# Optimization experiments

Hardware: AMD Instinct MI355X
Metric: run time of the kernel (lower is better)

## Reference

```python
import jax, jax.numpy as jnp
import numpy as np

B, N, D, H = 256, 64, 128, 64

def _w(key, shape, fan_in):
    return jax.random.normal(key, shape, jnp.float32) * (1.0 / np.sqrt(fan_in))

def setup_inputs() -> dict:
    key = jax.random.key(0)
    ks = jax.random.split(key, 6)
    return {
        "observations": jax.random.normal(ks[0], (B, N, D), jnp.float32),
        "enc_w": _w(ks[1], (D, H), D), "enc_b": jnp.zeros((H,), jnp.float32),
        "gate_w1": _w(ks[2], (2 * H, H), 2 * H), "gate_b1": jnp.zeros((H,), jnp.float32),
        "gate_w2": _w(ks[3], (H, 1), H), "gate_b2": jnp.zeros((1,), jnp.float32),
        "msg_w1": _w(ks[4], (H, H), H), "msg_b1": jnp.zeros((H,), jnp.float32),
        "msg_w2": _w(ks[5], (H, H), H), "msg_b2": jnp.zeros((H,), jnp.float32),
    }

def reference(observations, enc_w, enc_b, gate_w1, gate_b1, gate_w2, gate_b2,
              msg_w1, msg_b1, msg_w2, msg_b2):
    # encoder: (B, N, H)
    enc = jax.nn.relu(observations @ enc_w + enc_b)
    h = enc.shape[-1]
    # gate layer 1 on concat([e_i, e_j]) == e_i @ W_top + e_j @ W_bot; avoids
    # materializing the (B, N, N, 2H) concat tensor.
    w_i, w_j = gate_w1[:h], gate_w1[h:]
    gi = enc @ w_i                       # (B, N, H) contribution of receiver i
    gj = enc @ w_j + gate_b1             # (B, N, H) contribution of sender j
    hid = jax.nn.relu(gi[:, :, None, :] + gj[:, None, :, :])   # (B, N, N, H)
    gates = jax.nn.sigmoid(jnp.squeeze(hid @ gate_w2, -1) + gate_b2[0])  # (B, N, N)
    # message_gen(encoded): identical for every i in the original loop
    msg = jax.nn.relu(enc @ msg_w1 + msg_b1) @ msg_w2 + msg_b2  # (B, N, H)
    # enhanced[b, i] = sum_j gates[b, i, j] * msg[b, j]
    enhanced = jnp.einsum('bij,bjh->bih', gates, msg)           # (B, N, H)
    return enhanced
```

## Files before the change

kernel.cpp:

```cpp
#include <hip/hip_runtime.h>

typedef float  f32x4  __attribute__((ext_vector_type(4)));
typedef short  bf16x8 __attribute__((ext_vector_type(8)));

#define Bb 256

__device__ __forceinline__ uint cvtpk(float lo, float hi) {
    uint r;
    asm("v_cvt_pk_bf16_f32 %0, %1, %2" : "=v"(r) : "v"(lo), "v"(hi));
    return r;
}
__device__ __forceinline__ ushort f2b1(float v) { return (ushort)cvtpk(v, v); }
__device__ __forceinline__ float bflo(uint u) { return __uint_as_float(u << 16); }
__device__ __forceinline__ float bfhi(uint u) { return __uint_as_float(u & 0xffff0000u); }

__device__ __forceinline__ void gl_lds16(const void* g, void* l) {
    __builtin_amdgcn_global_load_lds(
        (const __attribute__((address_space(1))) unsigned int*)g,
        (__attribute__((address_space(3))) unsigned int*)l, 16, 0, 0);
}

union U8 { uint u[4]; bf16x8 v; };

__global__ __launch_bounds__(256) void gcm_prep(
    const float* __restrict__ obs, const float* __restrict__ enc_w,
    const float* __restrict__ gate_w1, const float* __restrict__ msg_w1,
    const float* __restrict__ msg_w2,
    ushort* __restrict__ obs_bf, ushort* __restrict__ wimg)
{
    const int bid = blockIdx.x, t = threadIdx.x;
    if (bid < 1024) {
        const int G  = bid * 256 + t;
        const int e0 = G * 8;
        const int b  = e0 >> 13;
        const int r  = (e0 >> 7) & 63;
        const int d0 = e0 & 127;
        const int ds = d0 ^ ((r & 7) << 3);
        const float* src = obs + (((size_t)b * 64 + r) * 128 + ds);
        float4 f0 = *(const float4*)src;
        float4 f1 = *(const float4*)(src + 4);
        uint4 o;
        o.x = cvtpk(f0.x, f0.y); o.y = cvtpk(f0.z, f0.w);
        o.z = cvtpk(f1.x, f1.y); o.w = cvtpk(f1.z, f1.w);
        *(uint4*)(obs_bf + e0) = o;
    } else {
        const int G  = (bid - 1024) * 256 + t;
        const int e0 = G * 8;
        float v[8];
        if (e0 < 8192) {
            const int n  = e0 >> 7;
            const int k0 = (e0 & 127) ^ ((n & 7) << 3);
            #pragma unroll
            for (int j = 0; j < 8; ++j) v[j] = enc_w[(k0 + j) * 64 + n];
        } else {
            const int e  = e0 - 8192;
            const int n  = e >> 6;
            const int k0 = (e & 63) ^ ((n & 7) << 3);
            const float* base; int col;
            if (n < 64)       { base = gate_w1;           col = n;       }
            else if (n < 128) { base = gate_w1 + 64 * 64; col = n - 64;  }
            else if (n < 192) { base = msg_w1;            col = n - 128; }
            else              { base = msg_w2;            col = n - 192; }
            #pragma unroll
            for (int j = 0; j < 8; ++j) v[j] = base[(k0 + j) * 64 + col];
        }
        uint4 o;
        o.x = cvtpk(v[0], v[1]); o.y = cvtpk(v[2], v[3]);
        o.z = cvtpk(v[4], v[5]); o.w = cvtpk(v[6], v[7]);
        *(uint4*)(wimg + e0) = o;
    }
}

__global__ __launch_bounds__(512, 4) void gcm_main(
    const ushort* __restrict__ obs_bf, const ushort* __restrict__ wimg,
    const float* __restrict__ enc_b, const float* __restrict__ gate_b1,
    const float* __restrict__ gate_w2, const float* __restrict__ gate_b2,
    const float* __restrict__ msg_b1, const float* __restrict__ msg_b2,
    ushort* __restrict__ gi_ws, float* __restrict__ out)
{
    const int bid  = blockIdx.x;
    const int bb   = bid >> 1;
    const int half = bid & 1;
    const int t    = threadIdx.x;
    const int lane = t & 63;
    const int wv   = t >> 6;
    const int lr   = lane & 15;
    const int lg   = lane >> 4;
    const int rt   = wv & 3;
    const int ch   = wv >> 2;

    __shared__ __align__(16) char arena[61440];
    ushort* s_wT     = (ushort*)(arena);
    ushort* s_enc    = (ushort*)(arena + 32768);
    ushort* s_msgT   = (ushort*)(arena + 32768);
    ushort* s_msgh   = (ushort*)(arena + 40960);
    ushort* s_gjb    = (ushort*)(arena + 49152);
    ushort* s_gatesb = (ushort*)(arena + 57344);

    #pragma unroll
    for (int i = 0; i < 4; ++i) {
        const int idx = wv * 4 + i;
        gl_lds16(wimg + 8192 + idx * 512 + lane * 8, arena + idx * 1024);
    }

    {
        const int arow = rt * 16 + lr;
        const ushort* ob = obs_bf + (size_t)bb * 8192 + arow * 128;
        bf16x8 a[4];
        #pragma unroll
        for (int ks = 0; ks < 4; ++ks)
            a[ks] = *(const bf16x8*)(ob + ((ks * 32 + lg * 8) ^ ((arow & 7) << 3)));
        f32x4 acc[2];
        acc[0] = (f32x4){0.f, 0.f, 0.f, 0.f};
        acc[1] = (f32x4){0.f, 0.f, 0.f, 0.f};
        #pragma unroll
        for (int jj = 0; jj < 2; ++jj) {
            const int n = ch * 32 + jj * 16 + lr;
            const ushort* wp = wimg + n * 128;
            #pragma unroll
            for (int ks = 0; ks < 4; ++ks) {
                bf16x8 bw = *(const bf16x8*)(wp + ((ks * 32 + lg * 8) ^ ((n & 7) << 3)));
                acc[jj] = __builtin_amdgcn_mfma_f32_16x16x32_bf16(a[ks], bw, acc[jj], 0, 0, 0);
            }
        }
        const int rb = rt * 16 + lg * 4;
        #pragma unroll
        for (int jj = 0; jj < 2; ++jj) {
            const int n = ch * 32 + jj * 16 + lr;
            const float be = enc_b[n];
            float v0 = fmaxf(acc[jj][0] + be, 0.f), v1 = fmaxf(acc[jj][1] + be, 0.f);
            float v2 = fmaxf(acc[jj][2] + be, 0.f), v3 = fmaxf(acc[jj][3] + be, 0.f);
            uint pA = cvtpk(v0, v1), pB = cvtpk(v2, v3);
            s_enc[((rb + 0) * 64 + n) ^ (((rb + 0) & 7) << 3)] = (ushort)pA;
            s_enc[((rb + 1) * 64 + n) ^ (((rb + 1) & 7) << 3)] = (ushort)(pA >> 16);
            s_enc[((rb + 2) * 64 + n) ^ (((rb + 2) & 7) << 3)] = (ushort)pB;
            s_enc[((rb + 3) * 64 + n) ^ (((rb + 3) & 7) << 3)] = (ushort)(pB >> 16);
        }
    }
    __syncthreads();

    {
        const int arow = rt * 16 + lr;
        bf16x8 a2[2];
        #pragma unroll
        for (int ks = 0; ks < 2; ++ks)
            a2[ks] = *(const bf16x8*)(s_enc + ((arow * 64 + ks * 32 + lg * 8) ^ ((arow & 7) << 3)));
        f32x4 acc[6];
        #pragma unroll
        for (int q = 0; q < 6; ++q) acc[q] = (f32x4){0.f, 0.f, 0.f, 0.f};
        #pragma unroll
        for (int q = 0; q < 6; ++q) {
            const int n = (ch * 6 + q) * 16 + lr;
            #pragma unroll
            for (int ks = 0; ks < 2; ++ks) {
                bf16x8 bw = *(const bf16x8*)(s_wT + ((n * 64 + ks * 32 + lg * 8) ^ ((n & 7) << 3)));
                acc[q] = __builtin_amdgcn_mfma_f32_16x16x32_bf16(a2[ks], bw, acc[q], 0, 0, 0);
            }
        }
        const int rb = rt * 16 + lg * 4;
        #pragma unroll
        for (int q = 0; q < 6; ++q) {
            const int nfull = (ch * 6 + q) * 16;
            const int cc = nfull + lr;
            if (nfull < 64) {
                if ((rt >> 1) == half) {
                    #pragma unroll
                    for (int rr = 0; rr < 4; ++rr)
                        gi_ws[(size_t)bb * 4096 + (rb + rr) * 64 + cc] = f2b1(acc[q][rr]);
                }
            } else if (nfull < 128) {
                const float b1 = gate_b1[cc - 64];
                #pragma unroll
                for (int rr = 0; rr < 4; ++rr) {
                    const int row = rb + rr;
                    s_gjb[(row * 64 + (cc - 64)) ^ ((row & 7) << 3)] = f2b1(acc[q][rr] + b1);
                }
            } else {
                const float bm = msg_b1[cc - 128];
                float v0 = fmaxf(acc[q][0] + bm, 0.f), v1 = fmaxf(acc[q][1] + bm, 0.f);
                float v2 = fmaxf(acc[q][2] + bm, 0.f), v3 = fmaxf(acc[q][3] + bm, 0.f);
                uint pA = cvtpk(v0, v1), pB = cvtpk(v2, v3);
                const int c2 = cc - 128;
                s_msgh[((rb + 0) * 64 + c2) ^ (((rb + 0) & 7) << 3)] = (ushort)pA;
                s_msgh[((rb + 1) * 64 + c2) ^ (((rb + 1) & 7) << 3)] = (ushort)(pA >> 16);
                s_msgh[((rb + 2) * 64 + c2) ^ (((rb + 2) & 7) << 3)] = (ushort)pB;
                s_msgh[((rb + 3) * 64 + c2) ^ (((rb + 3) & 7) << 3)] = (ushort)(pB >> 16);
            }
        }
    }
    __syncthreads();

    {
        const int arow = rt * 16 + lr;
        bf16x8 a3[2];
        #pragma unroll
        for (int ks = 0; ks < 2; ++ks)
            a3[ks] = *(const bf16x8*)(s_msgh + ((arow * 64 + ks * 32 + lg * 8) ^ ((arow & 7) << 3)));
        #pragma unroll
        for (int jj = 0; jj < 2; ++jj) {
            const int n = 192 + ch * 32 + jj * 16 + lr;
            f32x4 acc = (f32x4){0.f, 0.f, 0.f, 0.f};
            #pragma unroll
            for (int ks = 0; ks < 2; ++ks) {
                bf16x8 bw = *(const bf16x8*)(s_wT + ((n * 64 + ks * 32 + lg * 8) ^ ((n & 7) << 3)));
                acc = __builtin_amdgcn_mfma_f32_16x16x32_bf16(a3[ks], bw, acc, 0, 0, 0);
            }
            const int h  = ch * 32 + jj * 16 + lr;
            const int jb = rt * 16 + lg * 4;
            const float bm2 = msg_b2[h];
            uint pA = cvtpk(acc[0] + bm2, acc[1] + bm2);
            uint pB = cvtpk(acc[2] + bm2, acc[3] + bm2);
            const int e = (h * 64 + jb) ^ ((h & 7) << 3);
            *(uint*)(s_msgT + e)     = pA;
            *(uint*)(s_msgT + e + 2) = pB;
        }
    }

    {
        const int lrow0 = wv * 4;
        float gjv[64];
        #pragma unroll
        for (int c8 = 0; c8 < 8; ++c8) {
            uint4 p = *(const uint4*)(s_gjb + ((lane * 64 + c8 * 8) ^ ((lane & 7) << 3)));
            gjv[c8 * 8 + 0] = bflo(p.x); gjv[c8 * 8 + 1] = bfhi(p.x);
            gjv[c8 * 8 + 2] = bflo(p.y); gjv[c8 * 8 + 3] = bfhi(p.y);
            gjv[c8 * 8 + 4] = bflo(p.z); gjv[c8 * 8 + 5] = bfhi(p.z);
            gjv[c8 * 8 + 6] = bflo(p.w); gjv[c8 * 8 + 7] = bfhi(p.w);
        }
        const float b2v = gate_b2[0];
        #pragma unroll
        for (int r = 0; r < 4; ++r) {
            const int lrow = lrow0 + r;
            const int grow = __builtin_amdgcn_readfirstlane(half * 32 + lrow);
            const uint* gip = (const uint*)(gi_ws + (size_t)bb * 4096 + grow * 64);
            float acc = 0.f;
            #pragma unroll
            for (int c = 0; c < 32; ++c) {
                const uint p = gip[c];
                acc = fmaf(fmaxf(bflo(p) + gjv[2 * c],     0.f), gate_w2[2 * c],     acc);
                acc = fmaf(fmaxf(bfhi(p) + gjv[2 * c + 1], 0.f), gate_w2[2 * c + 1], acc);
            }
            const float g = 1.f / (1.f + __expf(-(acc + b2v)));
            s_gatesb[(lrow * 64 + lane) ^ ((lrow & 7) << 3)] = f2b1(g);
        }
    }
    __syncthreads();

    {
        const int rtl = wv >> 2;
        const int ctl = wv & 3;
        f32x4 acc = (f32x4){0.f, 0.f, 0.f, 0.f};
        const int arow = rtl * 16 + lr;
        const int n = ctl * 16 + lr;
        #pragma unroll
        for (int ks = 0; ks < 2; ++ks) {
            const int k0 = ks * 32 + lg * 8;
            bf16x8 a5 = *(const bf16x8*)(s_gatesb + ((arow * 64 + k0) ^ ((arow & 7) << 3)));
            bf16x8 b5 = *(const bf16x8*)(s_msgT   + ((n * 64 + k0) ^ ((n & 7) << 3)));
            acc = __builtin_amdgcn_mfma_f32_16x16x32_bf16(a5, b5, acc, 0, 0, 0);
        }
        const int rb = half * 32 + rtl * 16 + lg * 4;
        #pragma unroll
        for (int rr = 0; rr < 4; ++rr)
            out[((size_t)bb * 64 + rb + rr) * 64 + n] = acc[rr];
    }
}

__global__ __launch_bounds__(1024) void gcm_fb(
    const float* __restrict__ obs, const float* __restrict__ enc_w,
    const float* __restrict__ enc_b, const float* __restrict__ gate_w1,
    const float* __restrict__ gate_b1, const float* __restrict__ gate_w2,
    const float* __restrict__ gate_b2, const float* __restrict__ msg_w1,
    const float* __restrict__ msg_b1, const float* __restrict__ msg_w2,
    const float* __restrict__ msg_b2, float* __restrict__ out)
{
    const int bb   = blockIdx.x;
    const int t    = threadIdx.x;
    const int lane = t & 63;
    const int wv   = t >> 6;
    const int lr   = lane & 15;
    const int lg   = lane >> 4;
    const int rt   = wv & 3;
    const int ct   = wv >> 2;

    __shared__ __align__(16) ushort s_encwT[64 * 128];
    __shared__ __align__(16) ushort s_wT[256 * 64];
    __shared__ __align__(16) ushort s_enc[64 * 64];
    __shared__ __align__(16) ushort s_msgh[64 * 64];
    __shared__ __align__(16) ushort s_gatesb[64 * 64];
    __shared__ __align__(16) ushort s_msgT[64 * 64];
    __shared__ __align__(16) float  s_gi[64 * 64];
    __shared__ __align__(16) float  s_gj[64 * 64];
    __shared__ __align__(16) float  s_w2[64];

    float4 pf[8];
    {
        const float* ob = obs + ((size_t)bb * 64 + rt * 16 + lr) * 128 + lg * 8;
        #pragma unroll
        for (int ks = 0; ks < 4; ++ks) {
            pf[2 * ks]     = *(const float4*)(ob + ks * 32);
            pf[2 * ks + 1] = *(const float4*)(ob + ks * 32 + 4);
        }
    }
    if (t < 64) s_w2[t] = gate_w2[t];
    #pragma unroll
    for (int it = 0; it < 2; ++it) {
        const int g  = t + it * 1024;
        const int k  = g >> 4;
        const int n0 = (g & 15) * 4;
        float4 w4 = *(const float4*)(enc_w + k * 64 + n0);
        uint pA = cvtpk(w4.x, w4.y), pB = cvtpk(w4.z, w4.w);
        s_encwT[((n0 + 0) * 128 + k) ^ (((n0 + 0) & 7) << 3)] = (ushort)pA;
        s_encwT[((n0 + 1) * 128 + k) ^ (((n0 + 1) & 7) << 3)] = (ushort)(pA >> 16);
        s_encwT[((n0 + 2) * 128 + k) ^ (((n0 + 2) & 7) << 3)] = (ushort)pB;
        s_encwT[((n0 + 3) * 128 + k) ^ (((n0 + 3) & 7) << 3)] = (ushort)(pB >> 16);
    }
    bf16x8 afrag[4];
    #pragma unroll
    for (int ks = 0; ks < 4; ++ks) {
        U8 u;
        u.u[0] = cvtpk(pf[2 * ks].x,     pf[2 * ks].y);
        u.u[1] = cvtpk(pf[2 * ks].z,     pf[2 * ks].w);
        u.u[2] = cvtpk(pf[2 * ks + 1].x, pf[2 * ks + 1].y);
        u.u[3] = cvtpk(pf[2 * ks + 1].z, pf[2 * ks + 1].w);
        afrag[ks] = u.v;
    }
    float4 pfw[4];
    {
        const int k  = t >> 4;
        const int n0 = (t & 15) * 4;
        pfw[0] = *(const float4*)(gate_w1 + k * 64 + n0);
        pfw[1] = *(const float4*)(gate_w1 + (64 + k) * 64 + n0);
        pfw[2] = *(const float4*)(msg_w1 + k * 64 + n0);
        pfw[3] = *(const float4*)(msg_w2 + k * 64 + n0);
    }
    __syncthreads();
    {
        f32x4 acc = (f32x4){0.f, 0.f, 0.f, 0.f};
        const int n = ct * 16 + lr;
        #pragma unroll
        for (int ks = 0; ks < 4; ++ks) {
            const int k0 = ks * 32 + lg * 8;
            bf16x8 bf = *(const bf16x8*)(s_encwT + ((n * 128 + k0) ^ ((n & 7) << 3)));
            acc = __builtin_amdgcn_mfma_f32_16x16x32_bf16(afrag[ks], bf, acc, 0, 0, 0);
        }
        #pragma unroll
        for (int it = 0; it < 4; ++it) {
            const int k  = t >> 4;
            const int n0 = it * 64 + (t & 15) * 4;
            uint pA = cvtpk(pfw[it].x, pfw[it].y), pB = cvtpk(pfw[it].z, pfw[it].w);
            s_wT[((n0 + 0) * 64 + k) ^ (((n0 + 0) & 7) << 3)] = (ushort)pA;
            s_wT[((n0 + 1) * 64 + k) ^ (((n0 + 1) & 7) << 3)] = (ushort)(pA >> 16);
            s_wT[((n0 + 2) * 64 + k) ^ (((n0 + 2) & 7) << 3)] = (ushort)pB;
            s_wT[((n0 + 3) * 64 + k) ^ (((n0 + 3) & 7) << 3)] = (ushort)(pB >> 16);
        }
        const float be = enc_b[n];
        float v0 = fmaxf(acc[0] + be, 0.f), v1 = fmaxf(acc[1] + be, 0.f);
        float v2 = fmaxf(acc[2] + be, 0.f), v3 = fmaxf(acc[3] + be, 0.f);
        uint pA = cvtpk(v0, v1), pB = cvtpk(v2, v3);
        const int rb = rt * 16 + lg * 4;
        s_enc[((rb + 0) * 64 + n) ^ (((rb + 0) & 7) << 3)] = (ushort)pA;
        s_enc[((rb + 1) * 64 + n) ^ (((rb + 1) & 7) << 3)] = (ushort)(pA >> 16);
        s_enc[((rb + 2) * 64 + n) ^ (((rb + 2) & 7) << 3)] = (ushort)pB;
        s_enc[((rb + 3) * 64 + n) ^ (((rb + 3) & 7) << 3)] = (ushort)(pB >> 16);
    }
    __syncthreads();
    {
        f32x4 acc[3];
        #pragma unroll
        for (int q = 0; q < 3; ++q) acc[q] = (f32x4){0.f, 0.f, 0.f, 0.f};
        const int arow = rt * 16 + lr;
        #pragma unroll
        for (int ks = 0; ks < 2; ++ks) {
            const int k0 = ks * 32 + lg * 8;
            bf16x8 a = *(const bf16x8*)(s_enc + ((arow * 64 + k0) ^ ((arow & 7) << 3)));
            #pragma unroll
            for (int q = 0; q < 3; ++q) {
                const int n = (ct * 3 + q) * 16 + lr;
                bf16x8 bf = *(const bf16x8*)(s_wT + ((n * 64 + k0) ^ ((n & 7) << 3)));
                acc[q] = __builtin_amdgcn_mfma_f32_16x16x32_bf16(a, bf, acc[q], 0, 0, 0);
            }
        }
        const int rb = rt * 16 + lg * 4;
        #pragma unroll
        for (int q = 0; q < 3; ++q) {
            const int nfull = (ct * 3 + q) * 16;
            const int cc = nfull + lr;
            if (nfull < 64) {
                #pragma unroll
                for (int rr = 0; rr < 4; ++rr) {
                    const int row = rb + rr;
                    s_gi[(row * 64 + cc) ^ ((row & 7) << 2)] = acc[q][rr];
                }
            } else if (nfull < 128) {
                const float b1 = gate_b1[cc - 64];
                #pragma unroll
                for (int rr = 0; rr < 4; ++rr) {
                    const int row = rb + rr;
                    s_gj[(row * 64 + (cc - 64)) ^ ((row & 7) << 2)] = acc[q][rr] + b1;
                }
            } else {
                const float bm = msg_b1[cc - 128];
                float v0 = fmaxf(acc[q][0] + bm, 0.f), v1 = fmaxf(acc[q][1] + bm, 0.f);
                float v2 = fmaxf(acc[q][2] + bm, 0.f), v3 = fmaxf(acc[q][3] + bm, 0.f);
                uint pA = cvtpk(v0, v1), pB = cvtpk(v2, v3);
                const int c2 = cc - 128;
                s_msgh[((rb + 0) * 64 + c2) ^ (((rb + 0) & 7) << 3)] = (ushort)pA;
                s_msgh[((rb + 1) * 64 + c2) ^ (((rb + 1) & 7) << 3)] = (ushort)(pA >> 16);
                s_msgh[((rb + 2) * 64 + c2) ^ (((rb + 2) & 7) << 3)] = (ushort)pB;
                s_msgh[((rb + 3) * 64 + c2) ^ (((rb + 3) & 7) << 3)] = (ushort)(pB >> 16);
            }
        }
    }
    __syncthreads();
    {
        f32x4 acc = (f32x4){0.f, 0.f, 0.f, 0.f};
        const int arow = rt * 16 + lr;
        const int nn3 = 192 + ct * 16 + lr;
        #pragma unroll
        for (int ks = 0; ks < 2; ++ks) {
            const int k0 = ks * 32 + lg * 8;
            bf16x8 a = *(const bf16x8*)(s_msgh + ((arow * 64 + k0) ^ ((arow & 7) << 3)));
            bf16x8 bf = *(const bf16x8*)(s_wT + ((nn3 * 64 + k0) ^ ((nn3 & 7) << 3)));
            acc = __builtin_amdgcn_mfma_f32_16x16x32_bf16(a, bf, acc, 0, 0, 0);
        }
        const int h  = ct * 16 + lr;
        const int jb = rt * 16 + lg * 4;
        const float bm2 = msg_b2[h];
        uint pA = cvtpk(acc[0] + bm2, acc[1] + bm2);
        uint pB = cvtpk(acc[2] + bm2, acc[3] + bm2);
        const int e = (h * 64 + jb) ^ ((h & 7) << 3);
        *(uint*)(s_msgT + e)     = pA;
        *(uint*)(s_msgT + e + 2) = pB;
    }
    {
        const int row0g = wv * 4;
        float ag[4] = {0.f, 0.f, 0.f, 0.f};
        #pragma unroll 4
        for (int h0 = 0; h0 < 64; h0 += 4) {
            float4 gj4 = *(const float4*)&s_gj[(lane * 64 + h0) ^ ((lane & 7) << 2)];
            float4 w24 = *(const float4*)&s_w2[h0];
            #pragma unroll
            for (int r = 0; r < 4; ++r) {
                const int row = row0g + r;
                float4 gi4 = *(const float4*)&s_gi[(row * 64 + h0) ^ ((row & 7) << 2)];
                ag[r] = fmaf(fmaxf(gi4.x + gj4.x, 0.f), w24.x, ag[r]);
                ag[r] = fmaf(fmaxf(gi4.y + gj4.y, 0.f), w24.y, ag[r]);
                ag[r] = fmaf(fmaxf(gi4.z + gj4.z, 0.f), w24.z, ag[r]);
                ag[r] = fmaf(fmaxf(gi4.w + gj4.w, 0.f), w24.w, ag[r]);
            }
        }
        const float b2v = gate_b2[0];
        #pragma unroll
        for (int r = 0; r < 4; ++r) {
            const int row = row0g + r;
            const float g = 1.f / (1.f + __expf(-(ag[r] + b2v)));
            s_gatesb[(row * 64 + lane) ^ ((row & 7) << 3)] = f2b1(g);
        }
    }
    __syncthreads();
    {
        const int rtl = wv >> 2;
        const int ctl = wv & 3;
        f32x4 acc = (f32x4){0.f, 0.f, 0.f, 0.f};
        const int arow = rtl * 16 + lr;
        const int n = ctl * 16 + lr;
        #pragma unroll
        for (int ks = 0; ks < 2; ++ks) {
            const int k0 = ks * 32 + lg * 8;
            bf16x8 a  = *(const bf16x8*)(s_gatesb + ((arow * 64 + k0) ^ ((arow & 7) << 3)));
            bf16x8 bf = *(const bf16x8*)(s_msgT   + ((n * 64 + k0) ^ ((n & 7) << 3)));
            acc = __builtin_amdgcn_mfma_f32_16x16x32_bf16(a, bf, acc, 0, 0, 0);
        }
        const int rb = rtl * 16 + lg * 4;
        #pragma unroll
        for (int rr = 0; rr < 4; ++rr)
            out[((size_t)bb * 64 + rb + rr) * 64 + n] = acc[rr];
    }
}

extern "C" void kernel_launch(void* const* d_in, const int* in_sizes, int n_in,
                              void* d_out, int out_size, void* d_ws, size_t ws_size,
                              hipStream_t stream) {
    const float* obs     = (const float*)d_in[0];
    const float* enc_w   = (const float*)d_in[1];
    const float* enc_b   = (const float*)d_in[2];
    const float* gate_w1 = (const float*)d_in[3];
    const float* gate_b1 = (const float*)d_in[4];
    const float* gate_w2 = (const float*)d_in[5];
    const float* gate_b2 = (const float*)d_in[6];
    const float* msg_w1  = (const float*)d_in[7];
    const float* msg_b1  = (const float*)d_in[8];
    const float* msg_w2  = (const float*)d_in[9];
    const float* msg_b2  = (const float*)d_in[10];
    float* out = (float*)d_out;

    const size_t obs_elems = (size_t)Bb * 64 * 128;
    const size_t w_elems   = 24576;
    const size_t gi_elems  = (size_t)Bb * 64 * 64;
    const size_t need = (obs_elems + w_elems + gi_elems) * sizeof(ushort);
    if (ws_size >= need) {
        ushort* obs_bf = (ushort*)d_ws;
        ushort* wimg   = obs_bf + obs_elems;
        ushort* gi_ws  = wimg + w_elems;
        gcm_prep<<<1036, 256, 0, stream>>>(obs, enc_w, gate_w1, msg_w1, msg_w2,
                                           obs_bf, wimg);
        gcm_main<<<2 * Bb, 512, 0, stream>>>(obs_bf, wimg, enc_b, gate_b1,
                                             gate_w2, gate_b2, msg_b1, msg_b2,
                                             gi_ws, out);
    } else {
        gcm_fb<<<Bb, 1024, 0, stream>>>(obs, enc_w, enc_b, gate_w1, gate_b1,
                                        gate_w2, gate_b2, msg_w1, msg_b1,
                                        msg_w2, msg_b2, out);
    }
}
```

Measured before the change: 22.43 us.

## Restructure main kernel to one block per batch with wave-private row tiles

The main kernel now launches one 256-thread block per batch instead of two 512-thread half-blocks. Each wave owns 16 rows end to end, keeping intermediates in wave-private LDS. This removes the redundant per-half recompute, the global gi workspace round trip, the LDS weight staging, and all but one block barrier. Weights are now read straight from global memory/cache, each wave issues more MFMAs serially, and there are half as many blocks, which may reduce parallelism and latency hiding.

```diff
diff --git a/kernel.cpp b/kernel.cpp
--- a/kernel.cpp
+++ b/kernel.cpp
@@ -13,12 +13,6 @@
 __device__ __forceinline__ ushort f2b1(float v) { return (ushort)cvtpk(v, v); }
 __device__ __forceinline__ float bflo(uint u) { return __uint_as_float(u << 16); }
 __device__ __forceinline__ float bfhi(uint u) { return __uint_as_float(u & 0xffff0000u); }
-
-__device__ __forceinline__ void gl_lds16(const void* g, void* l) {
-    __builtin_amdgcn_global_load_lds(
-        (const __attribute__((address_space(1))) unsigned int*)g,
-        (__attribute__((address_space(3))) unsigned int*)l, 16, 0, 0);
-}
 
 union U8 { uint u[4]; bf16x8 v; };
 
@@ -71,142 +65,125 @@
     }
 }
 
-__global__ __launch_bounds__(512, 4) void gcm_main(
+__global__ __launch_bounds__(256) void gcm_main(
     const ushort* __restrict__ obs_bf, const ushort* __restrict__ wimg,
     const float* __restrict__ enc_b, const float* __restrict__ gate_b1,
     const float* __restrict__ gate_w2, const float* __restrict__ gate_b2,
     const float* __restrict__ msg_b1, const float* __restrict__ msg_b2,
-    ushort* __restrict__ gi_ws, float* __restrict__ out)
+    float* __restrict__ out)
 {
-    const int bid  = blockIdx.x;
-    const int bb   = bid >> 1;
-    const int half = bid & 1;
+    const int bb   = blockIdx.x;
     const int t    = threadIdx.x;
     const int lane = t & 63;
     const int wv   = t >> 6;
     const int lr   = lane & 15;
     const int lg   = lane >> 4;
-    const int rt   = wv & 3;
-    const int ch   = wv >> 2;
-
-    __shared__ __align__(16) char arena[61440];
-    ushort* s_wT     = (ushort*)(arena);
-    ushort* s_enc    = (ushort*)(arena + 32768);
-    ushort* s_msgT   = (ushort*)(arena + 32768);
-    ushort* s_msgh   = (ushort*)(arena + 40960);
-    ushort* s_gjb    = (ushort*)(arena + 49152);
-    ushort* s_gatesb = (ushort*)(arena + 57344);
-
-    #pragma unroll
-    for (int i = 0; i < 4; ++i) {
-        const int idx = wv * 4 + i;
-        gl_lds16(wimg + 8192 + idx * 512 + lane * 8, arena + idx * 1024);
-    }
-
-    {
-        const int arow = rt * 16 + lr;
+    const int R0   = wv * 16;
+
+    __shared__ __align__(16) char arena[41984];
+    ushort* s_pr1 = (ushort*)(arena)         + wv * 1024;
+    ushort* s_gi  = (ushort*)(arena + 8192)  + wv * 1024;
+    ushort* s_gat = (ushort*)(arena + 16384) + wv * 1024;
+    ushort* s_gjb  = (ushort*)(arena + 24576);
+    ushort* s_msgT = (ushort*)(arena + 33792);
+
+    {
+        const int arow = R0 + lr;
         const ushort* ob = obs_bf + (size_t)bb * 8192 + arow * 128;
         bf16x8 a[4];
         #pragma unroll
         for (int ks = 0; ks < 4; ++ks)
             a[ks] = *(const bf16x8*)(ob + ((ks * 32 + lg * 8) ^ ((arow & 7) << 3)));
-        f32x4 acc[2];
-        acc[0] = (f32x4){0.f, 0.f, 0.f, 0.f};
-        acc[1] = (f32x4){0.f, 0.f, 0.f, 0.f};
-        #pragma unroll
-        for (int jj = 0; jj < 2; ++jj) {
-            const int n = ch * 32 + jj * 16 + lr;
+        f32x4 acc[4];
+        #pragma unroll
+        for (int ct = 0; ct < 4; ++ct) acc[ct] = (f32x4){0.f, 0.f, 0.f, 0.f};
+        #pragma unroll
+        for (int ct = 0; ct < 4; ++ct) {
+            const int n = ct * 16 + lr;
             const ushort* wp = wimg + n * 128;
             #pragma unroll
             for (int ks = 0; ks < 4; ++ks) {
                 bf16x8 bw = *(const bf16x8*)(wp + ((ks * 32 + lg * 8) ^ ((n & 7) << 3)));
-                acc[jj] = __builtin_amdgcn_mfma_f32_16x16x32_bf16(a[ks], bw, acc[jj], 0, 0, 0);
-            }
-        }
-        const int rb = rt * 16 + lg * 4;
-        #pragma unroll
-        for (int jj = 0; jj < 2; ++jj) {
-            const int n = ch * 32 + jj * 16 + lr;
+                acc[ct] = __builtin_amdgcn_mfma_f32_16x16x32_bf16(a[ks], bw, acc[ct], 0, 0, 0);
+            }
+        }
+        #pragma unroll
+        for (int ct = 0; ct < 4; ++ct) {
+            const int n = ct * 16 + lr;
             const float be = enc_b[n];
-            float v0 = fmaxf(acc[jj][0] + be, 0.f), v1 = fmaxf(acc[jj][1] + be, 0.f);
-            float v2 = fmaxf(acc[jj][2] + be, 0.f), v3 = fmaxf(acc[jj][3] + be, 0.f);
-            uint pA = cvtpk(v0, v1), pB = cvtpk(v2, v3);
-            s_enc[((rb + 0) * 64 + n) ^ (((rb + 0) & 7) << 3)] = (ushort)pA;
-            s_enc[((rb + 1) * 64 + n) ^ (((rb + 1) & 7) << 3)] = (ushort)(pA >> 16);
-            s_enc[((rb + 2) * 64 + n) ^ (((rb + 2) & 7) << 3)] = (ushort)pB;
-            s_enc[((rb + 3) * 64 + n) ^ (((rb + 3) & 7) << 3)] = (ushort)(pB >> 16);
-        }
-    }
-    __syncthreads();
-
-    {
-        const int arow = rt * 16 + lr;
+            #pragma unroll
+            for (int rr = 0; rr < 4; ++rr) {
+                const int row = lg * 4 + rr;
+                float v = fmaxf(acc[ct][rr] + be, 0.f);
+                s_pr1[(row * 64 + n) ^ ((row & 7) << 3)] = f2b1(v);
+            }
+        }
+    }
+
+    {
         bf16x8 a2[2];
         #pragma unroll
         for (int ks = 0; ks < 2; ++ks)
-            a2[ks] = *(const bf16x8*)(s_enc + ((arow * 64 + ks * 32 + lg * 8) ^ ((arow & 7) << 3)));
-        f32x4 acc[6];
-        #pragma unroll
-        for (int q = 0; q < 6; ++q) acc[q] = (f32x4){0.f, 0.f, 0.f, 0.f};
-        #pragma unroll
-        for (int q = 0; q < 6; ++q) {
-            const int n = (ch * 6 + q) * 16 + lr;
+            a2[ks] = *(const bf16x8*)(s_pr1 + ((lr * 64 + ks * 32 + lg * 8) ^ ((lr & 7) << 3)));
+        f32x4 acc[12];
+        #pragma unroll
+        for (int q = 0; q < 12; ++q) acc[q] = (f32x4){0.f, 0.f, 0.f, 0.f};
+        #pragma unroll
+        for (int q = 0; q < 12; ++q) {
+            const int n = q * 16 + lr;
+            const ushort* wp = wimg + 8192 + n * 64;
             #pragma unroll
             for (int ks = 0; ks < 2; ++ks) {
-                bf16x8 bw = *(const bf16x8*)(s_wT + ((n * 64 + ks * 32 + lg * 8) ^ ((n & 7) << 3)));
+                bf16x8 bw = *(const bf16x8*)(wp + ((ks * 32 + lg * 8) ^ ((n & 7) << 3)));
                 acc[q] = __builtin_amdgcn_mfma_f32_16x16x32_bf16(a2[ks], bw, acc[q], 0, 0, 0);
             }
         }
-        const int rb = rt * 16 + lg * 4;
-        #pragma unroll
-        for (int q = 0; q < 6; ++q) {
-            const int nfull = (ch * 6 + q) * 16;
+        #pragma unroll
+        for (int q = 0; q < 12; ++q) {
+            const int nfull = q * 16;
             const int cc = nfull + lr;
             if (nfull < 64) {
-                if ((rt >> 1) == half) {
-                    #pragma unroll
-                    for (int rr = 0; rr < 4; ++rr)
-                        gi_ws[(size_t)bb * 4096 + (rb + rr) * 64 + cc] = f2b1(acc[q][rr]);
+                #pragma unroll
+                for (int rr = 0; rr < 4; ++rr) {
+                    const int row = lg * 4 + rr;
+                    s_gi[(row * 64 + cc) ^ ((row & 7) << 3)] = f2b1(acc[q][rr]);
                 }
             } else if (nfull < 128) {
                 const float b1 = gate_b1[cc - 64];
                 #pragma unroll
                 for (int rr = 0; rr < 4; ++rr) {
-                    const int row = rb + rr;
-                    s_gjb[(row * 64 + (cc - 64)) ^ ((row & 7) << 3)] = f2b1(acc[q][rr] + b1);
+                    const int grow = R0 + lg * 4 + rr;
+                    s_gjb[grow * 72 + (cc - 64)] = f2b1(acc[q][rr] + b1);
                 }
             } else {
                 const float bm = msg_b1[cc - 128];
-                float v0 = fmaxf(acc[q][0] + bm, 0.f), v1 = fmaxf(acc[q][1] + bm, 0.f);
-                float v2 = fmaxf(acc[q][2] + bm, 0.f), v3 = fmaxf(acc[q][3] + bm, 0.f);
-                uint pA = cvtpk(v0, v1), pB = cvtpk(v2, v3);
-                const int c2 = cc - 128;
-                s_msgh[((rb + 0) * 64 + c2) ^ (((rb + 0) & 7) << 3)] = (ushort)pA;
-                s_msgh[((rb + 1) * 64 + c2) ^ (((rb + 1) & 7) << 3)] = (ushort)(pA >> 16);
-                s_msgh[((rb + 2) * 64 + c2) ^ (((rb + 2) & 7) << 3)] = (ushort)pB;
-                s_msgh[((rb + 3) * 64 + c2) ^ (((rb + 3) & 7) << 3)] = (ushort)(pB >> 16);
-            }
-        }
-    }
-    __syncthreads();
-
-    {
-        const int arow = rt * 16 + lr;
+                #pragma unroll
+                for (int rr = 0; rr < 4; ++rr) {
+                    const int row = lg * 4 + rr;
+                    float v = fmaxf(acc[q][rr] + bm, 0.f);
+                    s_pr1[(row * 64 + (cc - 128)) ^ ((row & 7) << 3)] = f2b1(v);
+                }
+            }
+        }
+    }
+
+    {
         bf16x8 a3[2];
         #pragma unroll
         for (int ks = 0; ks < 2; ++ks)
-            a3[ks] = *(const bf16x8*)(s_msgh + ((arow * 64 + ks * 32 + lg * 8) ^ ((arow & 7) << 3)));
-        #pragma unroll
-        for (int jj = 0; jj < 2; ++jj) {
-            const int n = 192 + ch * 32 + jj * 16 + lr;
+            a3[ks] = *(const bf16x8*)(s_pr1 + ((lr * 64 + ks * 32 + lg * 8) ^ ((lr & 7) << 3)));
+        #pragma unroll
+        for (int jj = 0; jj < 4; ++jj) {
+            const int n = 192 + jj * 16 + lr;
+            const ushort* wp = wimg + 8192 + n * 64;
             f32x4 acc = (f32x4){0.f, 0.f, 0.f, 0.f};
             #pragma unroll
             for (int ks = 0; ks < 2; ++ks) {
-                bf16x8 bw = *(const bf16x8*)(s_wT + ((n * 64 + ks * 32 + lg * 8) ^ ((n & 7) << 3)));
+                bf16x8 bw = *(const bf16x8*)(wp + ((ks * 32 + lg * 8) ^ ((n & 7) << 3)));
                 acc = __builtin_amdgcn_mfma_f32_16x16x32_bf16(a3[ks], bw, acc, 0, 0, 0);
             }
-            const int h  = ch * 32 + jj * 16 + lr;
-            const int jb = rt * 16 + lg * 4;
+            const int h  = jj * 16 + lr;
+            const int jb = R0 + lg * 4;
             const float bm2 = msg_b2[h];
             uint pA = cvtpk(acc[0] + bm2, acc[1] + bm2);
             uint pB = cvtpk(acc[2] + bm2, acc[3] + bm2);
@@ -216,12 +193,13 @@
         }
     }
 
-    {
-        const int lrow0 = wv * 4;
+    __syncthreads();
+
+    {
         float gjv[64];
         #pragma unroll
         for (int c8 = 0; c8 < 8; ++c8) {
-            uint4 p = *(const uint4*)(s_gjb + ((lane * 64 + c8 * 8) ^ ((lane & 7) << 3)));
+            uint4 p = *(const uint4*)(s_gjb + lane * 72 + c8 * 8);
             gjv[c8 * 8 + 0] = bflo(p.x); gjv[c8 * 8 + 1] = bfhi(p.x);
             gjv[c8 * 8 + 2] = bflo(p.y); gjv[c8 * 8 + 3] = bfhi(p.y);
             gjv[c8 * 8 + 4] = bflo(p.z); gjv[c8 * 8 + 5] = bfhi(p.z);
@@ -229,40 +207,46 @@
         }
         const float b2v = gate_b2[0];
         #pragma unroll
-        for (int r = 0; r < 4; ++r) {
-            const int lrow = lrow0 + r;
-            const int grow = __builtin_amdgcn_readfirstlane(half * 32 + lrow);
-            const uint* gip = (const uint*)(gi_ws + (size_t)bb * 4096 + grow * 64);
+        for (int i = 0; i < 16; ++i) {
             float acc = 0.f;
             #pragma unroll
-            for (int c = 0; c < 32; ++c) {
-                const uint p = gip[c];
-                acc = fmaf(fmaxf(bflo(p) + gjv[2 * c],     0.f), gate_w2[2 * c],     acc);
-                acc = fmaf(fmaxf(bfhi(p) + gjv[2 * c + 1], 0.f), gate_w2[2 * c + 1], acc);
+            for (int c8 = 0; c8 < 8; ++c8) {
+                uint4 p = *(const uint4*)(s_gi + ((i * 64 + c8 * 8) ^ ((i & 7) << 3)));
+                const float* w2p = gate_w2 + c8 * 8;
+                acc = fmaf(fmaxf(bflo(p.x) + gjv[c8 * 8 + 0], 0.f), w2p[0], acc);
+                acc = fmaf(fmaxf(bfhi(p.x) + gjv[c8 * 8 + 1], 0.f), w2p[1], acc);
+                acc = fmaf(fmaxf(bflo(p.y) + gjv[c8 * 8 + 2], 0.f), w2p[2], acc);
+                acc = fmaf(fmaxf(bfhi(p.y) + gjv[c8 * 8 + 3], 0.f), w2p[3], acc);
+                acc = fmaf(fmaxf(bflo(p.z) + gjv[c8 * 8 + 4], 0.f), w2p[4], acc);
+                acc = fmaf(fmaxf(bfhi(p.z) + gjv[c8 * 8 + 5], 0.f), w2p[5], acc);
+                acc = fmaf(fmaxf(bflo(p.w) + gjv[c8 * 8 + 6], 0.f), w2p[6], acc);
+                acc = fmaf(fmaxf(bfhi(p.w) + gjv[c8 * 8 + 7], 0.f), w2p[7], acc);
             }
             const float g = 1.f / (1.f + __expf(-(acc + b2v)));
-            s_gatesb[(lrow * 64 + lane) ^ ((lrow & 7) << 3)] = f2b1(g);
-        }
-    }
-    __syncthreads();
-
-    {
-        const int rtl = wv >> 2;
-        const int ctl = wv & 3;
-        f32x4 acc = (f32x4){0.f, 0.f, 0.f, 0.f};
-        const int arow = rtl * 16 + lr;
-        const int n = ctl * 16 + lr;
-        #pragma unroll
-        for (int ks = 0; ks < 2; ++ks) {
-            const int k0 = ks * 32 + lg * 8;
-            bf16x8 a5 = *(const bf16x8*)(s_gatesb + ((arow * 64 + k0) ^ ((arow & 7) << 3)));
-            bf16x8 b5 = *(const bf16x8*)(s_msgT   + ((n * 64 + k0) ^ ((n & 7) << 3)));
-            acc = __builtin_amdgcn_mfma_f32_16x16x32_bf16(a5, b5, acc, 0, 0, 0);
-        }
-        const int rb = half * 32 + rtl * 16 + lg * 4;
-        #pragma unroll
-        for (int rr = 0; rr < 4; ++rr)
-            out[((size_t)bb * 64 + rb + rr) * 64 + n] = acc[rr];
+            s_gat[(i * 64 + lane) ^ ((i & 7) << 3)] = f2b1(g);
+        }
+    }
+
+    {
+        bf16x8 a5[2];
+        #pragma unroll
+        for (int ks = 0; ks < 2; ++ks)
+            a5[ks] = *(const bf16x8*)(s_gat + ((lr * 64 + ks * 32 + lg * 8) ^ ((lr & 7) << 3)));
+        #pragma unroll
+        for (int ctl = 0; ctl < 4; ++ctl) {
+            const int n = ctl * 16 + lr;
+            f32x4 acc = (f32x4){0.f, 0.f, 0.f, 0.f};
+            #pragma unroll
+            for (int ks = 0; ks < 2; ++ks) {
+                bf16x8 b5 = *(const bf16x8*)(s_msgT + ((n * 64 + ks * 32 + lg * 8) ^ ((n & 7) << 3)));
+                acc = __builtin_amdgcn_mfma_f32_16x16x32_bf16(a5[ks], b5, acc, 0, 0, 0);
+            }
+            #pragma unroll
+            for (int rr = 0; rr < 4; ++rr) {
+                const int grow = R0 + lg * 4 + rr;
+                out[((size_t)bb * 64 + grow) * 64 + n] = acc[rr];
+            }
+        }
     }
 }
 
@@ -497,17 +481,14 @@
 
     const size_t obs_elems = (size_t)Bb * 64 * 128;
     const size_t w_elems   = 24576;
-    const size_t gi_elems  = (size_t)Bb * 64 * 64;
-    const size_t need = (obs_elems + w_elems + gi_elems) * sizeof(ushort);
+    const size_t need = (obs_elems + w_elems) * sizeof(ushort);
     if (ws_size >= need) {
         ushort* obs_bf = (ushort*)d_ws;
         ushort* wimg   = obs_bf + obs_elems;
-        ushort* gi_ws  = wimg + w_elems;
         gcm_prep<<<1036, 256, 0, stream>>>(obs, enc_w, gate_w1, msg_w1, msg_w2,
                                            obs_bf, wimg);
-        gcm_main<<<2 * Bb, 512, 0, stream>>>(obs_bf, wimg, enc_b, gate_b1,
-                                             gate_w2, gate_b2, msg_b1, msg_b2,
-                                             gi_ws, out);
+        gcm_main<<<Bb, 256, 0, stream>>>(obs_bf, wimg, enc_b, gate_b1,
+                                         gate_w2, gate_b2, msg_b1, msg_b2, out);
     } else {
         gcm_fb<<<Bb, 1024, 0, stream>>>(obs, enc_w, enc_b, gate_w1, gate_b1,
                                         gate_w2, gate_b2, msg_w1, msg_b1,
```

After: 28.62 us. 27.6% more time.
